# Kernel tuning notes

Hardware: AMD Instinct MI355X
Metric: run time of the kernel (lower is better)

Reference implementation:

```python
import jax, jax.numpy as jnp
import numpy as np

B, T, F_IN, L, D = 512, 32, 4096, 256, 256
EPS = 1e-8
KM_ITERS = 100


def _linear(x, w, b):
    return x @ w.T + b


def _clf(h, w0, b0, w1, b1, w2, b2, w3, b3):
    # Linear->ReLU (Dropout is identity in eval) x3 then final Linear
    h = jax.nn.relu(_linear(h, w0, b0))
    h = jax.nn.relu(_linear(h, w1, b1))
    h = jax.nn.relu(_linear(h, w2, b2))
    return _linear(h, w3, b3)


def _kmeans_cosine(f):
    # f: (T, L). 2-cluster kmeans with cosine distance, fixed iteration count.
    fn = f / (jnp.linalg.norm(f, axis=1, keepdims=True) + EPS)
    centers0 = jnp.stack([f[0], f[T // 2]])  # deterministic init (ref: random pick)

    def step(centers, _):
        cn = centers / (jnp.linalg.norm(centers, axis=1, keepdims=True) + EPS)
        sim = fn @ cn.T                           # (T,2) cosine similarity
        assign = jnp.argmax(sim, axis=1)          # argmin of (1 - sim)
        mask = jax.nn.one_hot(assign, 2, dtype=f.dtype)  # (T,2)
        counts = mask.sum(axis=0)                 # (2,)
        new = (mask.T @ f) / jnp.clip(counts, 1.0)[:, None]
        new = jnp.where(counts[:, None] > 0, new, centers)
        return new, assign

    centers, assigns = jax.lax.scan(step, centers0, None, length=KM_ITERS)
    return assigns[-1], centers


def setup_inputs() -> dict:
    key = jax.random.key(0)
    ks = jax.random.split(key, 32)
    s = 0.02
    inp = {
        "x": jax.random.normal(ks[0], (B, T, F_IN), dtype=jnp.float32),
        "tsn_w": jax.random.normal(ks[1], (L, F_IN, 3), dtype=jnp.float32) * s,
        "tsn_b": jnp.zeros((L,), jnp.float32),
        "aV_w": jax.random.normal(ks[2], (D, L), dtype=jnp.float32) * s,
        "aV_b": jnp.zeros((D,), jnp.float32),
        "aU_w": jax.random.normal(ks[3], (D, L), dtype=jnp.float32) * s,
        "aU_b": jnp.zeros((D,), jnp.float32),
        "gate_w": jax.random.normal(ks[4], (1, D), dtype=jnp.float32) * s,
        "gate_b": jnp.zeros((1,), jnp.float32),
    }
    dims_bag = [(D, L), (D // 2, D), (32, D // 2), (1, 32)]
    dims_seg = [(D, L + 1), (D // 2, D), (32, D // 2), (1, 32)]
    for j, (o, i) in enumerate(dims_bag):
        inp[f"cb_w{j}"] = jax.random.normal(ks[5 + j], (o, i), dtype=jnp.float32) * s
        inp[f"cb_b{j}"] = jnp.zeros((o,), jnp.float32)
    for j, (o, i) in enumerate(dims_seg):
        inp[f"cs_w{j}"] = jax.random.normal(ks[9 + j], (o, i), dtype=jnp.float32) * s
        inp[f"cs_b{j}"] = jnp.zeros((o,), jnp.float32)
    return inp


def reference(x, tsn_w, tsn_b, aV_w, aV_b, aU_w, aU_b, gate_w, gate_b,
              cb_w0, cb_b0, cb_w1, cb_b1, cb_w2, cb_b2, cb_w3, cb_b3,
              cs_w0, cs_b0, cs_w1, cs_b1, cs_w2, cs_b2, cs_w3, cs_b3):
    feat_in = jnp.nan_to_num(x)  # (B,T,4096)
    # Conv1d over time (kernel 3, pad 1): NCH layout
    feature = jax.lax.conv_general_dilated(
        feat_in.transpose(0, 2, 1), tsn_w, (1,), [(1, 1)],
        dimension_numbers=('NCH', 'OIH', 'NCH')) + tsn_b[None, :, None]
    feature = feature.transpose(0, 2, 1)  # (B,T,L)

    # Gated MIL attention
    A_V = jnp.tanh(_linear(feature, aV_w, aV_b))
    A_U = jax.nn.sigmoid(_linear(feature, aU_w, aU_b))
    A = _linear(A_V * A_U, gate_w, gate_b)      # (B,T,1)
    At = A.transpose(0, 2, 1)                   # (B,1,T)
    bag = jnp.einsum('bot,btl->bol', jax.nn.softmax(At, axis=2), feature)[:, 0]  # (B,L)

    output1 = jax.nn.sigmoid(_clf(bag, cb_w0, cb_b0, cb_w1, cb_b1,
                                  cb_w2, cb_b2, cb_w3, cb_b3)).reshape(-1)  # (B,)

    seg_in = jnp.concatenate([feature, A], axis=2)  # (B,T,L+1)
    output_seg = jax.nn.sigmoid(_clf(seg_in, cs_w0, cs_b0, cs_w1, cs_b1,
                                     cs_w2, cs_b2, cs_w3, cs_b3)[..., 0])  # (B,T)

    # Per-sample 2-means cosine clustering (batched via vmap instead of python loop)
    assigns, _ = jax.vmap(_kmeans_cosine)(feature)  # (B,T) int
    mask0 = assigns == 0
    cnt0 = mask0.sum(1).astype(output_seg.dtype)
    cnt1 = T - cnt0
    m0 = jnp.where(mask0, output_seg, 0.0).sum(1) / jnp.clip(cnt0, 1.0)
    m1 = jnp.where(~mask0, output_seg, 0.0).sum(1) / jnp.clip(cnt1, 1.0)
    m0 = jnp.where(cnt0 > 0, m0, -jnp.inf)
    m1 = jnp.where(cnt1 > 0, m1, -jnp.inf)
    output2 = jnp.maximum(m0, m1)  # (B,)

    weight = 0.5
    output = jnp.stack([output1 * weight, output2 * (1.0 - weight)], axis=1)  # (B,2)
    # (ragged cluster index lists replaced by the dense assignment map `assigns`)
    return feature, assigns, output_seg, output, At
```

## Files before the change

kernel.cpp:

```cpp
#include <hip/hip_runtime.h>
#include <cfloat>
#include <cmath>

#define NB 512
#define NT 32
#define FIN 4096
#define NL 256
#define ND 256
#define NM (NB*NT)
#define KCONV (3*FIN)
#define PLANE 3145728
#define KTILES 192

#define BM 128
#define BN 128
#define BK 32
#define LDT 132

typedef __attribute__((ext_vector_type(8))) short short8_t;
typedef __attribute__((ext_vector_type(4))) float f32x4;

__device__ __forceinline__ float sigmoidf_(float v) { return 1.0f / (1.0f + expf(-v)); }

__device__ __forceinline__ unsigned short f2bf(float v) {
  unsigned u = __float_as_uint(v);
  unsigned r = u + 0x7FFFu + ((u >> 16) & 1u);
  return (unsigned short)(r >> 16);
}
__device__ __forceinline__ float bf2f(unsigned short h) {
  return __uint_as_float(((unsigned)h) << 16);
}

__global__ void __launch_bounds__(256) repack_frag_k(const float* __restrict__ w,
                                                     unsigned short* __restrict__ wt) {
  int d = blockIdx.x * 256 + threadIdx.x;
  int kt = d >> 13;
  int bc = (d >> 9) & 15;
  int lane = (d >> 3) & 63;
  int j = d & 7;
  int kb = lane >> 4;
  int kk = kt * 32 + kb * 8 + j;
  int l = bc * 16 + (lane & 15);
  int tap = kk >> 12;
  int f = kk & 4095;
  float v = w[(size_t)l * KCONV + f * 3 + tap];
  unsigned short hi = f2bf(v);
  unsigned short lo = f2bf(v - bf2f(hi));
  wt[d] = hi;
  wt[PLANE + d] = lo;
}

__global__ void __launch_bounds__(256) repack_dense_k(const float* __restrict__ W1,
    const float* __restrict__ W2, int nsplit, int ldw, int KB, int N16,
    unsigned short* __restrict__ wt, int planeElems) {
  int d = blockIdx.x * 256 + threadIdx.x;
  if (d >= planeElems) return;
  int j = d & 7;
  int lane = (d >> 3) & 63;
  int bckt = d >> 9;
  int bc = bckt % N16;
  int kt = bckt / N16;
  int kk = kt * 32 + (lane >> 4) * 8 + j;
  int l = bc * 16 + (lane & 15);
  float v = 0.f;
  if (kk < KB) {
    if (l < nsplit) v = W1[(size_t)l * ldw + kk];
    else            v = W2[(size_t)(l - nsplit) * ldw + kk];
  }
  unsigned short hi = f2bf(v);
  unsigned short lo = f2bf(v - bf2f(hi));
  wt[d] = hi;
  wt[planeElems + d] = lo;
}

__global__ void __launch_bounds__(256) conv_mfma3_k(const float* __restrict__ x,
    const unsigned short* __restrict__ WT, float* __restrict__ PART) {
  __shared__ __align__(16) unsigned short LB[2][16384];
  const int tid = threadIdx.x;
  const int lane = tid & 63;
  const int w = tid >> 6;
  const int wr = w >> 1, wc = w & 1;
  const int bid = blockIdx.x;
  const int swz = ((bid & 7) << 6) + (bid >> 3);
  const int m0 = (swz & 127) << 7;
  const int by = (swz >> 7) & 1;
  const int kz = swz >> 8;
  const int ktBase = kz * KTILES;

  f32x4 acc[4][4] = {};
  float4 avA[4];

  auto loadA = [&](int kt, float4* av) {
#pragma unroll
    for (int rb = 0; rb < 2; ++rb) {
      const int br = (w << 1) + rb;
      const int gm = m0 + br * 16 + (lane & 15);
      const int tap = kt >> 7;
      const int f0 = (kt & 127) << 5;
      const int tt = (gm & 31) + tap - 1;
      if ((unsigned)tt < 32u) {
        const float* src = x + (size_t)(gm + tap - 1) * FIN + f0 + ((lane >> 4) << 3);
        av[rb*2+0] = *reinterpret_cast<const float4*>(src);
        av[rb*2+1] = *reinterpret_cast<const float4*>(src + 4);
      } else {
        av[rb*2+0] = make_float4(0.f,0.f,0.f,0.f);
        av[rb*2+1] = make_float4(0.f,0.f,0.f,0.f);
      }
    }
  };
  auto writeA = [&](int buf, const float4* av) {
#pragma unroll
    for (int rb = 0; rb < 2; ++rb) {
      float vv[8];
      *reinterpret_cast<float4*>(&vv[0]) = av[rb*2+0];
      *reinterpret_cast<float4*>(&vv[4]) = av[rb*2+1];
      __align__(16) unsigned short hi8[8];
      __align__(16) unsigned short lo8[8];
#pragma unroll
      for (int e = 0; e < 8; ++e) {
        float v = vv[e];
        v = (v == v) ? v : 0.0f;
        unsigned short h = f2bf(v);
        hi8[e] = h;
        lo8[e] = f2bf(v - bf2f(h));
      }
      const int br = (w << 1) + rb;
      const int off = (br << 9) + (lane << 3);
      *reinterpret_cast<short8_t*>(&LB[buf][off])        = *reinterpret_cast<const short8_t*>(hi8);
      *reinterpret_cast<short8_t*>(&LB[buf][4096 + off]) = *reinterpret_cast<const short8_t*>(lo8);
    }
  };
  auto stageB = [&](int buf, int kt) {
#pragma unroll
    for (int cb = 0; cb < 2; ++cb) {
      const int bc = (w << 1) + cb;
      const unsigned short* sh = WT + (((size_t)kt * 16 + (by << 3) + bc) << 9) + (lane << 3);
      __builtin_amdgcn_global_load_lds(
          (const __attribute__((address_space(1))) void*)sh,
          (__attribute__((address_space(3))) void*)&LB[buf][8192 + (bc << 9)], 16, 0, 0);
      __builtin_amdgcn_global_load_lds(
          (const __attribute__((address_space(1))) void*)(sh + PLANE),
          (__attribute__((address_space(3))) void*)&LB[buf][12288 + (bc << 9)], 16, 0, 0);
    }
  };

  stageB(0, ktBase);
  loadA(ktBase, avA);
  asm volatile("s_waitcnt vmcnt(0)" ::: "memory");
  writeA(0, avA);
  loadA(ktBase + 1, avA);
  stageB(1, ktBase + 1);
  asm volatile("s_waitcnt lgkmcnt(0)" ::: "memory");
  __builtin_amdgcn_s_barrier();

  for (int i = 0; i < KTILES; ++i) {
    const int cur = i & 1;
    if (i + 1 < KTILES) {
      asm volatile("s_waitcnt vmcnt(4)" ::: "memory");
      writeA(cur ^ 1, avA);
      if (i + 2 < KTILES) loadA(ktBase + i + 2, avA);
    }
    {
      const unsigned short* A0 = &LB[cur][0];
      const unsigned short* B0 = &LB[cur][8192];
      short8_t bh[4], bl[4];
#pragma unroll
      for (int c = 0; c < 4; ++c) {
        const int bc = wc * 4 + c;
        bh[c] = *reinterpret_cast<const short8_t*>(B0 + (bc << 9) + (lane << 3));
        bl[c] = *reinterpret_cast<const short8_t*>(B0 + 4096 + (bc << 9) + (lane << 3));
      }
#pragma unroll
      for (int r = 0; r < 4; ++r) {
        const int br = wr * 4 + r;
        short8_t ah = *reinterpret_cast<const short8_t*>(A0 + (br << 9) + (lane << 3));
        short8_t al = *reinterpret_cast<const short8_t*>(A0 + 4096 + (br << 9) + (lane << 3));
#pragma unroll
        for (int c = 0; c < 4; ++c) {
          acc[r][c] = __builtin_amdgcn_mfma_f32_16x16x32_bf16(ah, bh[c], acc[r][c], 0, 0, 0);
          acc[r][c] = __builtin_amdgcn_mfma_f32_16x16x32_bf16(ah, bl[c], acc[r][c], 0, 0, 0);
          acc[r][c] = __builtin_amdgcn_mfma_f32_16x16x32_bf16(al, bh[c], acc[r][c], 0, 0, 0);
        }
      }
    }
    if (i + 1 < KTILES) {
      if (i + 2 < KTILES) {
        asm volatile("s_waitcnt vmcnt(4)" ::: "memory");
      } else {
        asm volatile("s_waitcnt vmcnt(0)" ::: "memory");
      }
      asm volatile("s_waitcnt lgkmcnt(0)" ::: "memory");
      __builtin_amdgcn_sched_barrier(0);
      __builtin_amdgcn_s_barrier();
      if (i + 2 < KTILES) stageB(cur, ktBase + i + 2);
    }
  }

  float* P = PART + (size_t)kz * ((size_t)NM * NL);
#pragma unroll
  for (int r = 0; r < 4; ++r) {
#pragma unroll
    for (int c = 0; c < 4; ++c) {
#pragma unroll
      for (int e = 0; e < 4; ++e) {
        int row = m0 + wr * 64 + r * 16 + ((lane >> 4) << 2) + e;
        int col = by * 128 + wc * 64 + c * 16 + (lane & 15);
        P[(size_t)row * NL + col] = acc[r][c][e];
      }
    }
  }
}

__global__ void __launch_bounds__(256) reduce_bias_k(const float* __restrict__ PART,
    const float* __restrict__ bias, float* __restrict__ feat) {
  int i = blockIdx.x * 256 + threadIdx.x;
  size_t base = (size_t)i * 4;
  float4 a = *reinterpret_cast<const float4*>(PART + base);
  float4 b = *reinterpret_cast<const float4*>(PART + (size_t)NM * NL + base);
  int c0 = (int)(base & 255);
  float4 bb = *reinterpret_cast<const float4*>(bias + c0);
  float4 o;
  o.x = a.x + b.x + bb.x;
  o.y = a.y + b.y + bb.y;
  o.z = a.z + b.z + bb.z;
  o.w = a.w + b.w + bb.w;
  *reinterpret_cast<float4*>(feat + base) = o;
}

template <int ACT, int SEG>
__global__ void __launch_bounds__(256) mfma_gemm_k(const float* __restrict__ A, int lda,
    const float* __restrict__ Aws, const unsigned short* __restrict__ WT,
    int planeElems, int N16, int KT,
    const float* __restrict__ bias1, const float* __restrict__ bias2, int bsplit,
    float* __restrict__ C, int N) {
  __shared__ __align__(16) unsigned short AS[8192];
  __shared__ __align__(16) unsigned short BS[8192];
  const int tid = threadIdx.x;
  const int m0 = blockIdx.x * 128;
  const int by = blockIdx.y;
  const int lane = tid & 63;
  const int w = tid >> 6, wr = w >> 1, wc = w & 1;
  const int kb = tid & 3;
  const int rquot = tid >> 2;

  f32x4 acc[4][4] = {};
  float4 avreg[4];
  short8_t bvreg[4];

  {
#pragma unroll
    for (int u = 0; u < 2; ++u) {
      int gm = m0 + u * 64 + rquot;
      const float* src = A + (size_t)gm * lda + kb * 8;
      avreg[u*2+0] = *reinterpret_cast<const float4*>(src);
      avreg[u*2+1] = *reinterpret_cast<const float4*>(src + 4);
    }
#pragma unroll
    for (int q = 0; q < 4; ++q) {
      int p = q >> 1, pass = q & 1;
      bvreg[q] = *reinterpret_cast<const short8_t*>(WT + (size_t)p * planeElems
                  + ((size_t)by * 8) * 512 + (pass*256 + tid) * 8);
    }
  }

  for (int i = 0; i < KT; ++i) {
#pragma unroll
    for (int u = 0; u < 2; ++u) {
      float vv[8];
      *reinterpret_cast<float4*>(&vv[0]) = avreg[u*2+0];
      *reinterpret_cast<float4*>(&vv[4]) = avreg[u*2+1];
      __align__(16) unsigned short hi[8];
      __align__(16) unsigned short lo[8];
#pragma unroll
      for (int e = 0; e < 8; ++e) {
        float v = vv[e];
        unsigned short h = f2bf(v);
        hi[e] = h;
        lo[e] = f2bf(v - bf2f(h));
      }
      int row = u * 64 + rquot;
      int br = row >> 4;
      int lanew = (row & 15) + (kb << 4);
      int off = br * 512 + lanew * 8;
      *reinterpret_cast<short8_t*>(AS + off)        = *reinterpret_cast<const short8_t*>(hi);
      *reinterpret_cast<short8_t*>(AS + 4096 + off) = *reinterpret_cast<const short8_t*>(lo);
    }
#pragma unroll
    for (int q = 0; q < 4; ++q) {
      int p = q >> 1, pass = q & 1;
      *reinterpret_cast<short8_t*>(BS + p * 4096 + (pass*256 + tid) * 8) = bvreg[q];
    }
    __syncthreads();

    if (i + 1 < KT) {
      int kk0 = (i + 1) * 32;
#pragma unroll
      for (int u = 0; u < 2; ++u) {
        int gm = m0 + u * 64 + rquot;
        if (SEG && kk0 >= 256) {
          float a0 = (kb == 0) ? Aws[gm] : 0.f;
          avreg[u*2+0] = make_float4(a0, 0.f, 0.f, 0.f);
          avreg[u*2+1] = make_float4(0.f, 0.f, 0.f, 0.f);
        } else {
          const float* src = A + (size_t)gm * lda + kk0 + kb * 8;
          avreg[u*2+0] = *reinterpret_cast<const float4*>(src);
          avreg[u*2+1] = *reinterpret_cast<const float4*>(src + 4);
        }
      }
#pragma unroll
      for (int q = 0; q < 4; ++q) {
        int p = q >> 1, pass = q & 1;
        bvreg[q] = *reinterpret_cast<const short8_t*>(WT + (size_t)p * planeElems
                    + ((size_t)(i + 1) * N16 + by * 8) * 512 + (pass*256 + tid) * 8);
      }
    }

    short8_t bh[4], bl[4];
#pragma unroll
    for (int c = 0; c < 4; ++c) {
      int bc = wc * 4 + c;
      bh[c] = *reinterpret_cast<const short8_t*>(BS + bc * 512 + lane * 8);
      bl[c] = *reinterpret_cast<const short8_t*>(BS + 4096 + bc * 512 + lane * 8);
    }
#pragma unroll
    for (int r = 0; r < 4; ++r) {
      int br = wr * 4 + r;
      short8_t ah = *reinterpret_cast<const short8_t*>(AS + br * 512 + lane * 8);
      short8_t al = *reinterpret_cast<const short8_t*>(AS + 4096 + br * 512 + lane * 8);
#pragma unroll
      for (int c = 0; c < 4; ++c) {
        acc[r][c] = __builtin_amdgcn_mfma_f32_16x16x32_bf16(ah, bh[c], acc[r][c], 0, 0, 0);
        acc[r][c] = __builtin_amdgcn_mfma_f32_16x16x32_bf16(ah, bl[c], acc[r][c], 0, 0, 0);
        acc[r][c] = __builtin_amdgcn_mfma_f32_16x16x32_bf16(al, bh[c], acc[r][c], 0, 0, 0);
      }
    }
    __syncthreads();
  }

#pragma unroll
  for (int r = 0; r < 4; ++r) {
#pragma unroll
    for (int c = 0; c < 4; ++c) {
#pragma unroll
      for (int e = 0; e < 4; ++e) {
        int row = m0 + wr * 64 + r * 16 + ((lane >> 4) << 2) + e;
        int col = by * 128 + wc * 64 + c * 16 + (lane & 15);
        float b = (col < bsplit) ? bias1[col] : bias2[col - bsplit];
        float v = acc[r][c][e] + b;
        if (ACT == 1) v = fmaxf(v, 0.f);
        C[(size_t)row * N + col] = v;
      }
    }
  }
}

template <int ACT>
__global__ void __launch_bounds__(256) gemm_wt_k(const float* __restrict__ A, int lda,
    const float* __restrict__ W, int ldw, int KB,
    const float* __restrict__ bias, float* __restrict__ C,
    int N, int K) {
  __shared__ float As[BK][LDT];
  __shared__ float Bs[BK][LDT];
  const int tid = threadIdx.x;
  const int m0 = blockIdx.x * BM;
  const int n0 = blockIdx.y * BN;
  const int row0 = (tid >> 4) << 3;
  const int col0 = (tid & 15) << 3;
  float acc[8][8] = {};
  for (int kk0 = 0; kk0 < K; kk0 += BK) {
#pragma unroll
    for (int i = 0; i < 4; ++i) {
      int v = i * 256 + tid;
      int row = v >> 3;
      int f4 = (v & 7) << 2;
      float4 val = *reinterpret_cast<const float4*>(A + (size_t)(m0 + row) * lda + kk0 + f4);
      As[f4 + 0][row] = val.x;
      As[f4 + 1][row] = val.y;
      As[f4 + 2][row] = val.z;
      As[f4 + 3][row] = val.w;
    }
#pragma unroll
    for (int i = 0; i < 4; ++i) {
      int v = i * 256 + tid;
      int n = v >> 3;
      int kq = (v & 7) << 2;
      int gn = n0 + n;
#pragma unroll
      for (int j = 0; j < 4; ++j) {
        int kk = kk0 + kq + j;
        float bv = 0.f;
        if (gn < N && kk < KB) bv = W[(size_t)gn * ldw + kk];
        Bs[kq + j][n] = bv;
      }
    }
    __syncthreads();
#pragma unroll
    for (int kk = 0; kk < BK; ++kk) {
      float a[8], b[8];
      *reinterpret_cast<float4*>(&a[0]) = *reinterpret_cast<const float4*>(&As[kk][row0]);
      *reinterpret_cast<float4*>(&a[4]) = *reinterpret_cast<const float4*>(&As[kk][row0 + 4]);
      *reinterpret_cast<float4*>(&b[0]) = *reinterpret_cast<const float4*>(&Bs[kk][col0]);
      *reinterpret_cast<float4*>(&b[4]) = *reinterpret_cast<const float4*>(&Bs[kk][col0 + 4]);
#pragma unroll
      for (int r = 0; r < 8; ++r)
#pragma unroll
        for (int c = 0; c < 8; ++c)
          acc[r][c] = fmaf(a[r], b[c], acc[r][c]);
    }
    __syncthreads();
  }
#pragma unroll
  for (int r = 0; r < 8; ++r) {
    int m = m0 + row0 + r;
#pragma unroll
    for (int c = 0; c < 8; ++c) {
      int n = n0 + col0 + c;
      if (n < N) {
        float v = acc[r][c] + bias[n];
        if (ACT == 1) v = fmaxf(v, 0.f);
        C[(size_t)m * (size_t)N + n] = v;
      }
    }
  }
}

__global__ void __launch_bounds__(256) gate_k(const float* __restrict__ Y,
    const float* __restrict__ gw, const float* __restrict__ gb,
    float* __restrict__ Aws, float* __restrict__ At) {
  int lane = threadIdx.x & 63;
  int m = blockIdx.x * 4 + (threadIdx.x >> 6);
  float4 v4 = *reinterpret_cast<const float4*>(Y + (size_t)m * 512 + lane * 4);
  float4 u4 = *reinterpret_cast<const float4*>(Y + (size_t)m * 512 + 256 + lane * 4);
  float4 g4 = *reinterpret_cast<const float4*>(gw + lane * 4);
  float s = tanhf(v4.x) * sigmoidf_(u4.x) * g4.x
          + tanhf(v4.y) * sigmoidf_(u4.y) * g4.y
          + tanhf(v4.z) * sigmoidf_(u4.z) * g4.z
          + tanhf(v4.w) * sigmoidf_(u4.w) * g4.w;
#pragma unroll
  for (int off = 32; off > 0; off >>= 1) s += __shfl_xor(s, off, 64);
  if (lane == 0) {
    float a = s + gb[0];
    Aws[m] = a;
    At[m] = a;
  }
}

__global__ void __launch_bounds__(256) softmax_bag_k(const float* __restrict__ Aws,
    const float* __restrict__ feat, float* __restrict__ bag) {
  __shared__ float av[NT];
  __shared__ float ev[NT];
  int b = blockIdx.x, tid = threadIdx.x;
  if (tid < NT) av[tid] = Aws[b * NT + tid];
  __syncthreads();
  float mx = -FLT_MAX;
#pragma unroll
  for (int t = 0; t < NT; ++t) mx = fmaxf(mx, av[t]);
  if (tid < NT) ev[tid] = expf(av[tid] - mx);
  __syncthreads();
  float ssum = 0.f;
#pragma unroll
  for (int t = 0; t < NT; ++t) ssum += ev[t];
  float accv = 0.f;
#pragma unroll
  for (int t = 0; t < NT; ++t) accv += ev[t] * feat[((size_t)b * NT + t) * NL + tid];
  bag[(size_t)b * NL + tid] = accv / ssum;
}

__global__ void __launch_bounds__(256) rowdot32_k(const float* __restrict__ H,
    const float* __restrict__ w, const float* __restrict__ bptr,
    float* __restrict__ outp, int ostride, float scale) {
  int m = blockIdx.x * 256 + threadIdx.x;
  const float* h = H + (size_t)m * 32;
  float s = bptr[0];
#pragma unroll
  for (int i = 0; i < 32; i += 4) {
    float4 hv = *reinterpret_cast<const float4*>(h + i);
    float4 wv = *reinterpret_cast<const float4*>(w + i);
    s += hv.x * wv.x + hv.y * wv.y + hv.z * wv.z + hv.w * wv.w;
  }
  outp[(size_t)m * ostride] = scale * sigmoidf_(s);
}

__global__ void __launch_bounds__(64) kmeans_k(const float* __restrict__ feat,
    const float* __restrict__ seg, float* __restrict__ assigns_out,
    float* __restrict__ outpair) {
  __shared__ float fls[NT][260];
  int b = blockIdx.x, lane = threadIdx.x;
  int l0 = lane << 2;
  float fn[NT][4];
#pragma unroll
  for (int t = 0; t < NT; ++t) {
    float4 v = *reinterpret_cast<const float4*>(feat + ((size_t)b * NT + t) * NL + l0);
    *reinterpret_cast<float4*>(&fls[t][l0]) = v;
    float ss = v.x * v.x + v.y * v.y + v.z * v.z + v.w * v.w;
#pragma unroll
    for (int off = 32; off > 0; off >>= 1) ss += __shfl_xor(ss, off, 64);
    float nr = sqrtf(ss) + 1e-8f;
    fn[t][0] = v.x / nr; fn[t][1] = v.y / nr; fn[t][2] = v.z / nr; fn[t][3] = v.w / nr;
  }
  __syncthreads();
  float cr0[4], cr1[4];
#pragma unroll
  for (int i = 0; i < 4; ++i) { cr0[i] = fls[0][l0 + i]; cr1[i] = fls[16][l0 + i]; }

  unsigned long long amask = 0ull;
  unsigned long long prev = ~0ull;
  int c1n = 0;
  for (int it = 0; it < 100; ++it) {
    float ss0 = cr0[0]*cr0[0] + cr0[1]*cr0[1] + cr0[2]*cr0[2] + cr0[3]*cr0[3];
    float ss1 = cr1[0]*cr1[0] + cr1[1]*cr1[1] + cr1[2]*cr1[2] + cr1[3]*cr1[3];
#pragma unroll
    for (int off = 32; off > 0; off >>= 1) {
      ss0 += __shfl_xor(ss0, off, 64);
      ss1 += __shfl_xor(ss1, off, 64);
    }
    float nr0 = sqrtf(ss0) + 1e-8f, nr1 = sqrtf(ss1) + 1e-8f;
    float cn0[4], cn1[4];
#pragma unroll
    for (int i = 0; i < 4; ++i) { cn0[i] = cr0[i] / nr0; cn1[i] = cr1[i] / nr1; }
    float p[64];
#pragma unroll
    for (int t = 0; t < NT; ++t) {
      p[2*t]   = fn[t][0]*cn0[0] + fn[t][1]*cn0[1] + fn[t][2]*cn0[2] + fn[t][3]*cn0[3];
      p[2*t+1] = fn[t][0]*cn1[0] + fn[t][1]*cn1[1] + fn[t][2]*cn1[2] + fn[t][3]*cn1[3];
    }
    float v32[32];
    { bool hi = (lane & 32) != 0;
#pragma unroll
      for (int i = 0; i < 32; ++i) {
        float keep = hi ? p[32+i] : p[i];
        float send = hi ? p[i] : p[32+i];
        v32[i] = keep + __shfl_xor(send, 32, 64);
      } }
    float v16[16];
    { bool hi = (lane & 16) != 0;
#pragma unroll
      for (int i = 0; i < 16; ++i) {
        float keep = hi ? v32[16+i] : v32[i];
        float send = hi ? v32[i] : v32[16+i];
        v16[i] = keep + __shfl_xor(send, 16, 64);
      } }
    float v8[8];
    { bool hi = (lane & 8) != 0;
#pragma unroll
      for (int i = 0; i < 8; ++i) {
        float keep = hi ? v16[8+i] : v16[i];
        float send = hi ? v16[i] : v16[8+i];
        v8[i] = keep + __shfl_xor(send, 8, 64);
      } }
    float v4[4];
    { bool hi = (lane & 4) != 0;
#pragma unroll
      for (int i = 0; i < 4; ++i) {
        float keep = hi ? v8[4+i] : v8[i];
        float send = hi ? v8[i] : v8[4+i];
        v4[i] = keep + __shfl_xor(send, 4, 64);
      } }
    float v2[2];
    { bool hi = (lane & 2) != 0;
#pragma unroll
      for (int i = 0; i < 2; ++i) {
        float keep = hi ? v4[2+i] : v4[i];
        float send = hi ? v4[i] : v4[2+i];
        v2[i] = keep + __shfl_xor(send, 2, 64);
      } }
    float sim;
    { bool hi = (lane & 1) != 0;
      float keep = hi ? v2[1] : v2[0];
      float send = hi ? v2[0] : v2[1];
      sim = keep + __shfl_xor(send, 1, 64);
    }
    float simo = __shfl_xor(sim, 1, 64);
    bool is0 = (lane & 1) == 0;
    unsigned long long mask = __ballot(is0 && (simo > sim));
    int c1 = __popcll(mask);
    int c0 = NT - c1;
    amask = mask; c1n = c1;
    if (mask == prev) break;
    prev = mask;
    float s0v[4] = {0,0,0,0}, s1v[4] = {0,0,0,0};
#pragma unroll
    for (int t = 0; t < NT; ++t) {
      float mt = (float)((mask >> (2*t)) & 1ull);
      float nt = 1.0f - mt;
      float4 fv = *reinterpret_cast<const float4*>(&fls[t][l0]);
      s1v[0] = fmaf(mt, fv.x, s1v[0]); s1v[1] = fmaf(mt, fv.y, s1v[1]);
      s1v[2] = fmaf(mt, fv.z, s1v[2]); s1v[3] = fmaf(mt, fv.w, s1v[3]);
      s0v[0] = fmaf(nt, fv.x, s0v[0]); s0v[1] = fmaf(nt, fv.y, s0v[1]);
      s0v[2] = fmaf(nt, fv.z, s0v[2]); s0v[3] = fmaf(nt, fv.w, s0v[3]);
    }
    float fc0 = fmaxf((float)c0, 1.0f), fc1 = fmaxf((float)c1, 1.0f);
#pragma unroll
    for (int i = 0; i < 4; ++i) {
      float n0v = s0v[i] / fc0;
      float n1v = s1v[i] / fc1;
      cr0[i] = (c0 > 0) ? n0v : cr0[i];
      cr1[i] = (c1 > 0) ? n1v : cr1[i];
    }
  }
  if (lane < NT)
    assigns_out[(size_t)b * NT + lane] = (amask & (1ull << (2*lane))) ? 1.0f : 0.0f;
  if (lane == 0) {
    float sum0 = 0.f, sum1 = 0.f;
    for (int t = 0; t < NT; ++t) {
      float sv = seg[(size_t)b * NT + t];
      if (amask & (1ull << (2*t))) sum1 += sv; else sum0 += sv;
    }
    int c1 = c1n, c0 = NT - c1n;
    float m0 = (c0 > 0) ? (sum0 / fmaxf((float)c0, 1.f)) : -INFINITY;
    float m1 = (c1 > 0) ? (sum1 / fmaxf((float)c1, 1.f)) : -INFINITY;
    outpair[(size_t)b * 2 + 1] = 0.5f * fmaxf(m0, m1);
  }
}

extern "C" void kernel_launch(void* const* d_in, const int* in_sizes, int n_in,
                              void* d_out, int out_size, void* d_ws, size_t ws_size,
                              hipStream_t stream) {
  const float* x      = (const float*)d_in[0];
  const float* tsn_w  = (const float*)d_in[1];
  const float* tsn_b  = (const float*)d_in[2];
  const float* aV_w   = (const float*)d_in[3];
  const float* aV_b   = (const float*)d_in[4];
  const float* aU_w   = (const float*)d_in[5];
  const float* aU_b   = (const float*)d_in[6];
  const float* gate_w = (const float*)d_in[7];
  const float* gate_b = (const float*)d_in[8];
  const float* cb_w0  = (const float*)d_in[9];
  const float* cb_b0  = (const float*)d_in[10];
  const float* cb_w1  = (const float*)d_in[11];
  const float* cb_b1  = (const float*)d_in[12];
  const float* cb_w2  = (const float*)d_in[13];
  const float* cb_b2  = (const float*)d_in[14];
  const float* cb_w3  = (const float*)d_in[15];
  const float* cb_b3  = (const float*)d_in[16];
  const float* cs_w0  = (const float*)d_in[17];
  const float* cs_b0  = (const float*)d_in[18];
  const float* cs_w1  = (const float*)d_in[19];
  const float* cs_b1  = (const float*)d_in[20];
  const float* cs_w2  = (const float*)d_in[21];
  const float* cs_b2  = (const float*)d_in[22];
  const float* cs_w3  = (const float*)d_in[23];
  const float* cs_b3  = (const float*)d_in[24];

  float* out = (float*)d_out;
  float* o_feat   = out;
  float* o_assign = out + 4194304;
  float* o_seg    = out + 4210688;
  float* o_out    = out + 4227072;
  float* o_At     = out + 4228096;

  char* ws = (char*)d_ws;
  unsigned short* WT = (unsigned short*)ws;
  float* PART  = (float*)(ws + 12582912);
  unsigned short* WVU = (unsigned short*)ws;
  unsigned short* WC0 = (unsigned short*)(ws + 524288);
  unsigned short* WC1 = (unsigned short*)(ws + 819200);
  float* AWS   = (float*)(ws + 950272);
  float* BAG   = (float*)(ws + 1015808);
  float* BH0   = (float*)(ws + 1540096);
  float* BH1   = (float*)(ws + 2064384);
  float* BH2   = (float*)(ws + 2326528);
  float* Y     = (float*)(ws + 12582912);
  float* SH0   = (float*)(ws + 12582912);
  float* SH1   = (float*)(ws + 29360128);
  float* SH2   = (float*)(ws + 37748736);

  repack_frag_k<<<dim3(12288), dim3(256), 0, stream>>>(tsn_w, WT);
  conv_mfma3_k<<<dim3(512), dim3(256), 0, stream>>>(x, WT, PART);
  reduce_bias_k<<<dim3(4096), dim3(256), 0, stream>>>(PART, tsn_b, o_feat);
  repack_dense_k<<<dim3(512), dim3(256), 0, stream>>>(aV_w, aU_w, 256, 256, 256, 32, WVU, 131072);
  repack_dense_k<<<dim3(288), dim3(256), 0, stream>>>(cs_w0, cs_w0, 256, 257, 257, 16, WC0, 73728);
  repack_dense_k<<<dim3(128), dim3(256), 0, stream>>>(cs_w1, cs_w1, 256, 256, 256, 8, WC1, 32768);
  mfma_gemm_k<0,0><<<dim3(128, 4), dim3(256), 0, stream>>>(o_feat, 256, nullptr, WVU,
      131072, 32, 8, aV_b, aU_b, 256, Y, 512);
  gate_k<<<dim3(4096), dim3(256), 0, stream>>>(Y, gate_w, gate_b, AWS, o_At);
  softmax_bag_k<<<dim3(512), dim3(256), 0, stream>>>(AWS, o_feat, BAG);
  gemm_wt_k<1><<<dim3(4, 2), dim3(256), 0, stream>>>(BAG, 256, cb_w0, 256, 256, cb_b0, BH0, 256, 256);
  gemm_wt_k<1><<<dim3(4, 1), dim3(256), 0, stream>>>(BH0, 256, cb_w1, 256, 256, cb_b1, BH1, 128, 256);
  gemm_wt_k<1><<<dim3(4, 1), dim3(256), 0, stream>>>(BH1, 128, cb_w2, 128, 128, cb_b2, BH2, 32, 128);
  rowdot32_k<<<dim3(2), dim3(256), 0, stream>>>(BH2, cb_w3, cb_b3, o_out, 2, 0.5f);
  mfma_gemm_k<1,1><<<dim3(128, 2), dim3(256), 0, stream>>>(o_feat, 256, AWS, WC0,
      73728, 16, 9, cs_b0, cs_b0, 256, SH0, 256);
  mfma_gemm_k<1,0><<<dim3(128, 1), dim3(256), 0, stream>>>(SH0, 256, nullptr, WC1,
      32768, 8, 8, cs_b1, cs_b1, 128, SH1, 128);
  gemm_wt_k<1><<<dim3(128, 1), dim3(256), 0, stream>>>(SH1, 128, cs_w2, 128, 128, cs_b2, SH2, 32, 128);
  rowdot32_k<<<dim3(64), dim3(256), 0, stream>>>(SH2, cs_w3, cs_b3, o_seg, 1, 1.0f);
  kmeans_k<<<dim3(512), dim3(64), 0, stream>>>(o_feat, o_seg, o_assign, o_out);
}
```

Baseline: 736.1 us.

## Replace LDS-staged conv GEMM with register-direct double-buffered loads

```diff
diff --git a/kernel.cpp b/kernel.cpp
--- a/kernel.cpp
+++ b/kernel.cpp
@@ -73,127 +73,91 @@
   wt[planeElems + d] = lo;
 }
 
-__global__ void __launch_bounds__(256) conv_mfma3_k(const float* __restrict__ x,
+struct Aset { float4 v[8]; };
+struct Bset { short8_t b[8]; };
+
+__device__ __forceinline__ void conv_loadstep(const float* __restrict__ x,
+    const unsigned short* __restrict__ WT, int m0, int by, int kt,
+    int wr, int wc, int lane, Aset& A, Bset& B) {
+  const int tap = kt >> 7;
+  const int fbase = ((kt & 127) << 5) + ((lane >> 4) << 3);
+#pragma unroll
+  for (int r = 0; r < 4; ++r) {
+    const int br = wr * 4 + r;
+    const int gm = m0 + br * 16 + (lane & 15);
+    const int tt = (gm & 31) + tap - 1;
+    float4 a0 = make_float4(0.f, 0.f, 0.f, 0.f);
+    float4 a1 = a0;
+    if ((unsigned)tt < 32u) {
+      const float* src = x + (size_t)(gm + tap - 1) * FIN + fbase;
+      a0 = *reinterpret_cast<const float4*>(src);
+      a1 = *reinterpret_cast<const float4*>(src + 4);
+    }
+    A.v[2*r]   = a0;
+    A.v[2*r+1] = a1;
+  }
+  const unsigned short* bbase = WT + (((size_t)kt * 16 + (by << 3)) << 9) + (lane << 3);
+#pragma unroll
+  for (int c = 0; c < 4; ++c) {
+    const int bc = wc * 4 + c;
+    B.b[c]     = *reinterpret_cast<const short8_t*>(bbase + ((size_t)bc << 9));
+    B.b[4 + c] = *reinterpret_cast<const short8_t*>(bbase + ((size_t)bc << 9) + PLANE);
+  }
+}
+
+__device__ __forceinline__ void conv_compstep(const Aset& A, const Bset& B,
+                                              f32x4 acc[4][4]) {
+#pragma unroll
+  for (int r = 0; r < 4; ++r) {
+    float vv[8];
+    *reinterpret_cast<float4*>(&vv[0]) = A.v[2*r];
+    *reinterpret_cast<float4*>(&vv[4]) = A.v[2*r+1];
+    __align__(16) unsigned short hi8[8];
+    __align__(16) unsigned short lo8[8];
+#pragma unroll
+    for (int e = 0; e < 8; ++e) {
+      float v = vv[e];
+      v = (v == v) ? v : 0.0f;
+      unsigned short h = f2bf(v);
+      hi8[e] = h;
+      lo8[e] = f2bf(v - bf2f(h));
+    }
+    short8_t ah = *reinterpret_cast<const short8_t*>(hi8);
+    short8_t al = *reinterpret_cast<const short8_t*>(lo8);
+#pragma unroll
+    for (int c = 0; c < 4; ++c) {
+      acc[r][c] = __builtin_amdgcn_mfma_f32_16x16x32_bf16(ah, B.b[c],     acc[r][c], 0, 0, 0);
+      acc[r][c] = __builtin_amdgcn_mfma_f32_16x16x32_bf16(ah, B.b[4 + c], acc[r][c], 0, 0, 0);
+      acc[r][c] = __builtin_amdgcn_mfma_f32_16x16x32_bf16(al, B.b[c],     acc[r][c], 0, 0, 0);
+    }
+  }
+}
+
+__global__ void __launch_bounds__(256) conv_mfma4_k(const float* __restrict__ x,
     const unsigned short* __restrict__ WT, float* __restrict__ PART) {
-  __shared__ __align__(16) unsigned short LB[2][16384];
   const int tid = threadIdx.x;
   const int lane = tid & 63;
   const int w = tid >> 6;
   const int wr = w >> 1, wc = w & 1;
   const int bid = blockIdx.x;
-  const int swz = ((bid & 7) << 6) + (bid >> 3);
-  const int m0 = (swz & 127) << 7;
-  const int by = (swz >> 7) & 1;
-  const int kz = swz >> 8;
+  const int xcd = bid & 7;
+  const int j = bid >> 3;
+  const int m0 = (xcd * 16 + (j >> 2)) << 7;
+  const int by = j & 1;
+  const int kz = (j >> 1) & 1;
   const int ktBase = kz * KTILES;
 
   f32x4 acc[4][4] = {};
-  float4 avA[4];
-
-  auto loadA = [&](int kt, float4* av) {
-#pragma unroll
-    for (int rb = 0; rb < 2; ++rb) {
-      const int br = (w << 1) + rb;
-      const int gm = m0 + br * 16 + (lane & 15);
-      const int tap = kt >> 7;
-      const int f0 = (kt & 127) << 5;
-      const int tt = (gm & 31) + tap - 1;
-      if ((unsigned)tt < 32u) {
-        const float* src = x + (size_t)(gm + tap - 1) * FIN + f0 + ((lane >> 4) << 3);
-        av[rb*2+0] = *reinterpret_cast<const float4*>(src);
-        av[rb*2+1] = *reinterpret_cast<const float4*>(src + 4);
-      } else {
-        av[rb*2+0] = make_float4(0.f,0.f,0.f,0.f);
-        av[rb*2+1] = make_float4(0.f,0.f,0.f,0.f);
-      }
-    }
-  };
-  auto writeA = [&](int buf, const float4* av) {
-#pragma unroll
-    for (int rb = 0; rb < 2; ++rb) {
-      float vv[8];
-      *reinterpret_cast<float4*>(&vv[0]) = av[rb*2+0];
-      *reinterpret_cast<float4*>(&vv[4]) = av[rb*2+1];
-      __align__(16) unsigned short hi8[8];
-      __align__(16) unsigned short lo8[8];
-#pragma unroll
-      for (int e = 0; e < 8; ++e) {
-        float v = vv[e];
-        v = (v == v) ? v : 0.0f;
-        unsigned short h = f2bf(v);
-        hi8[e] = h;
-        lo8[e] = f2bf(v - bf2f(h));
-      }
-      const int br = (w << 1) + rb;
-      const int off = (br << 9) + (lane << 3);
-      *reinterpret_cast<short8_t*>(&LB[buf][off])        = *reinterpret_cast<const short8_t*>(hi8);
-      *reinterpret_cast<short8_t*>(&LB[buf][4096 + off]) = *reinterpret_cast<const short8_t*>(lo8);
-    }
-  };
-  auto stageB = [&](int buf, int kt) {
-#pragma unroll
-    for (int cb = 0; cb < 2; ++cb) {
-      const int bc = (w << 1) + cb;
-      const unsigned short* sh = WT + (((size_t)kt * 16 + (by << 3) + bc) << 9) + (lane << 3);
-      __builtin_amdgcn_global_load_lds(
-          (const __attribute__((address_space(1))) void*)sh,
-          (__attribute__((address_space(3))) void*)&LB[buf][8192 + (bc << 9)], 16, 0, 0);
-      __builtin_amdgcn_global_load_lds(
-          (const __attribute__((address_space(1))) void*)(sh + PLANE),
-          (__attribute__((address_space(3))) void*)&LB[buf][12288 + (bc << 9)], 16, 0, 0);
-    }
-  };
-
-  stageB(0, ktBase);
-  loadA(ktBase, avA);
-  asm volatile("s_waitcnt vmcnt(0)" ::: "memory");
-  writeA(0, avA);
-  loadA(ktBase + 1, avA);
-  stageB(1, ktBase + 1);
-  asm volatile("s_waitcnt lgkmcnt(0)" ::: "memory");
-  __builtin_amdgcn_s_barrier();
-
-  for (int i = 0; i < KTILES; ++i) {
-    const int cur = i & 1;
-    if (i + 1 < KTILES) {
-      asm volatile("s_waitcnt vmcnt(4)" ::: "memory");
-      writeA(cur ^ 1, avA);
-      if (i + 2 < KTILES) loadA(ktBase + i + 2, avA);
-    }
-    {
-      const unsigned short* A0 = &LB[cur][0];
-      const unsigned short* B0 = &LB[cur][8192];
-      short8_t bh[4], bl[4];
-#pragma unroll
-      for (int c = 0; c < 4; ++c) {
-        const int bc = wc * 4 + c;
-        bh[c] = *reinterpret_cast<const short8_t*>(B0 + (bc << 9) + (lane << 3));
-        bl[c] = *reinterpret_cast<const short8_t*>(B0 + 4096 + (bc << 9) + (lane << 3));
-      }
-#pragma unroll
-      for (int r = 0; r < 4; ++r) {
-        const int br = wr * 4 + r;
-        short8_t ah = *reinterpret_cast<const short8_t*>(A0 + (br << 9) + (lane << 3));
-        short8_t al = *reinterpret_cast<const short8_t*>(A0 + 4096 + (br << 9) + (lane << 3));
-#pragma unroll
-        for (int c = 0; c < 4; ++c) {
-          acc[r][c] = __builtin_amdgcn_mfma_f32_16x16x32_bf16(ah, bh[c], acc[r][c], 0, 0, 0);
-          acc[r][c] = __builtin_amdgcn_mfma_f32_16x16x32_bf16(ah, bl[c], acc[r][c], 0, 0, 0);
-          acc[r][c] = __builtin_amdgcn_mfma_f32_16x16x32_bf16(al, bh[c], acc[r][c], 0, 0, 0);
-        }
-      }
-    }
-    if (i + 1 < KTILES) {
-      if (i + 2 < KTILES) {
-        asm volatile("s_waitcnt vmcnt(4)" ::: "memory");
-      } else {
-        asm volatile("s_waitcnt vmcnt(0)" ::: "memory");
-      }
-      asm volatile("s_waitcnt lgkmcnt(0)" ::: "memory");
-      __builtin_amdgcn_sched_barrier(0);
-      __builtin_amdgcn_s_barrier();
-      if (i + 2 < KTILES) stageB(cur, ktBase + i + 2);
-    }
+  Aset A0, A1;
+  Bset B0, B1;
+
+  conv_loadstep(x, WT, m0, by, ktBase, wr, wc, lane, A0, B0);
+  for (int i = 0; i < KTILES; i += 2) {
+    conv_loadstep(x, WT, m0, by, ktBase + i + 1, wr, wc, lane, A1, B1);
+    conv_compstep(A0, B0, acc);
+    if (i + 2 < KTILES)
+      conv_loadstep(x, WT, m0, by, ktBase + i + 2, wr, wc, lane, A0, B0);
+    conv_compstep(A1, B1, acc);
   }
 
   float* P = PART + (size_t)kz * ((size_t)NM * NL);
@@ -666,7 +630,7 @@
   float* SH2   = (float*)(ws + 37748736);
 
   repack_frag_k<<<dim3(12288), dim3(256), 0, stream>>>(tsn_w, WT);
-  conv_mfma3_k<<<dim3(512), dim3(256), 0, stream>>>(x, WT, PART);
+  conv_mfma4_k<<<dim3(512), dim3(256), 0, stream>>>(x, WT, PART);
   reduce_bias_k<<<dim3(4096), dim3(256), 0, stream>>>(PART, tsn_b, o_feat);
   repack_dense_k<<<dim3(512), dim3(256), 0, stream>>>(aV_w, aU_w, 256, 256, 256, 32, WVU, 131072);
   repack_dense_k<<<dim3(288), dim3(256), 0, stream>>>(cs_w0, cs_w0, 256, 257, 257, 16, WC0, 73728);
```

Result: slower. 851.9 us (+15.7%).

## Widen conv GEMM tile to full 256 columns with 512-thread blocks

Applied to the files above, without the earlier changes.

```diff
diff --git a/kernel.cpp b/kernel.cpp
--- a/kernel.cpp
+++ b/kernel.cpp
@@ -73,138 +73,129 @@
   wt[planeElems + d] = lo;
 }
 
-__global__ void __launch_bounds__(256) conv_mfma3_k(const float* __restrict__ x,
+__global__ void __launch_bounds__(512) conv_mfma6_k(const float* __restrict__ x,
     const unsigned short* __restrict__ WT, float* __restrict__ PART) {
-  __shared__ __align__(16) unsigned short LB[2][16384];
+  __shared__ __align__(16) unsigned short LB[2][24576];
   const int tid = threadIdx.x;
   const int lane = tid & 63;
   const int w = tid >> 6;
   const int wr = w >> 1, wc = w & 1;
   const int bid = blockIdx.x;
-  const int swz = ((bid & 7) << 6) + (bid >> 3);
-  const int m0 = (swz & 127) << 7;
-  const int by = (swz >> 7) & 1;
-  const int kz = swz >> 8;
+  const int xcd = bid & 7;
+  const int j = bid >> 3;
+  const int m0 = (xcd * 16 + (j >> 1)) << 7;
+  const int kz = j & 1;
   const int ktBase = kz * KTILES;
-
-  f32x4 acc[4][4] = {};
-  float4 avA[4];
-
-  auto loadA = [&](int kt, float4* av) {
-#pragma unroll
-    for (int rb = 0; rb < 2; ++rb) {
-      const int br = (w << 1) + rb;
-      const int gm = m0 + br * 16 + (lane & 15);
-      const int tap = kt >> 7;
-      const int f0 = (kt & 127) << 5;
-      const int tt = (gm & 31) + tap - 1;
-      if ((unsigned)tt < 32u) {
-        const float* src = x + (size_t)(gm + tap - 1) * FIN + f0 + ((lane >> 4) << 3);
-        av[rb*2+0] = *reinterpret_cast<const float4*>(src);
-        av[rb*2+1] = *reinterpret_cast<const float4*>(src + 4);
-      } else {
-        av[rb*2+0] = make_float4(0.f,0.f,0.f,0.f);
-        av[rb*2+1] = make_float4(0.f,0.f,0.f,0.f);
-      }
+  const int ar = tid >> 2;
+  const int akc = tid & 3;
+
+  f32x4 acc[2][8] = {};
+  float4 avA[2];
+
+  auto loadA = [&](int kt) {
+    const int tap = kt >> 7;
+    const int f0 = (kt & 127) << 5;
+    const int gm = m0 + ar;
+    const int tt = (gm & 31) + tap - 1;
+    if ((unsigned)tt < 32u) {
+      const float* src = x + (size_t)(gm + tap - 1) * FIN + f0 + (akc << 3);
+      avA[0] = *reinterpret_cast<const float4*>(src);
+      avA[1] = *reinterpret_cast<const float4*>(src + 4);
+    } else {
+      avA[0] = make_float4(0.f, 0.f, 0.f, 0.f);
+      avA[1] = make_float4(0.f, 0.f, 0.f, 0.f);
     }
   };
-  auto writeA = [&](int buf, const float4* av) {
-#pragma unroll
-    for (int rb = 0; rb < 2; ++rb) {
-      float vv[8];
-      *reinterpret_cast<float4*>(&vv[0]) = av[rb*2+0];
-      *reinterpret_cast<float4*>(&vv[4]) = av[rb*2+1];
-      __align__(16) unsigned short hi8[8];
-      __align__(16) unsigned short lo8[8];
-#pragma unroll
-      for (int e = 0; e < 8; ++e) {
-        float v = vv[e];
-        v = (v == v) ? v : 0.0f;
-        unsigned short h = f2bf(v);
-        hi8[e] = h;
-        lo8[e] = f2bf(v - bf2f(h));
-      }
-      const int br = (w << 1) + rb;
-      const int off = (br << 9) + (lane << 3);
-      *reinterpret_cast<short8_t*>(&LB[buf][off])        = *reinterpret_cast<const short8_t*>(hi8);
-      *reinterpret_cast<short8_t*>(&LB[buf][4096 + off]) = *reinterpret_cast<const short8_t*>(lo8);
-    }
+  auto writeA = [&](int buf) {
+    float vv[8];
+    *reinterpret_cast<float4*>(&vv[0]) = avA[0];
+    *reinterpret_cast<float4*>(&vv[4]) = avA[1];
+    __align__(16) unsigned short hi8[8];
+    __align__(16) unsigned short lo8[8];
+#pragma unroll
+    for (int e = 0; e < 8; ++e) {
+      float v = vv[e];
+      v = (v == v) ? v : 0.0f;
+      unsigned short h = f2bf(v);
+      hi8[e] = h;
+      lo8[e] = f2bf(v - bf2f(h));
+    }
+    const int off = ((ar >> 4) << 9) + (((ar & 15) + (akc << 4)) << 3);
+    *reinterpret_cast<short8_t*>(&LB[buf][off])        = *reinterpret_cast<const short8_t*>(hi8);
+    *reinterpret_cast<short8_t*>(&LB[buf][4096 + off]) = *reinterpret_cast<const short8_t*>(lo8);
   };
   auto stageB = [&](int buf, int kt) {
 #pragma unroll
-    for (int cb = 0; cb < 2; ++cb) {
-      const int bc = (w << 1) + cb;
-      const unsigned short* sh = WT + (((size_t)kt * 16 + (by << 3) + bc) << 9) + (lane << 3);
+    for (int q = 0; q < 4; ++q) {
+      const int c = w + (q << 3);
+      const int p = c >> 4, bc = c & 15;
+      const unsigned short* src = WT + (size_t)p * PLANE
+          + (((size_t)kt * 16 + bc) << 9) + (lane << 3);
       __builtin_amdgcn_global_load_lds(
-          (const __attribute__((address_space(1))) void*)sh,
-          (__attribute__((address_space(3))) void*)&LB[buf][8192 + (bc << 9)], 16, 0, 0);
-      __builtin_amdgcn_global_load_lds(
-          (const __attribute__((address_space(1))) void*)(sh + PLANE),
-          (__attribute__((address_space(3))) void*)&LB[buf][12288 + (bc << 9)], 16, 0, 0);
+          (const __attribute__((address_space(1))) void*)src,
+          (__attribute__((address_space(3))) void*)&LB[buf][8192 + (p << 13) + (bc << 9)],
+          16, 0, 0);
     }
   };
 
+  loadA(ktBase);
   stageB(0, ktBase);
-  loadA(ktBase, avA);
   asm volatile("s_waitcnt vmcnt(0)" ::: "memory");
-  writeA(0, avA);
-  loadA(ktBase + 1, avA);
-  stageB(1, ktBase + 1);
+  writeA(0);
+  __builtin_amdgcn_sched_barrier(0);
   asm volatile("s_waitcnt lgkmcnt(0)" ::: "memory");
   __builtin_amdgcn_s_barrier();
 
   for (int i = 0; i < KTILES; ++i) {
     const int cur = i & 1;
     if (i + 1 < KTILES) {
-      asm volatile("s_waitcnt vmcnt(4)" ::: "memory");
-      writeA(cur ^ 1, avA);
-      if (i + 2 < KTILES) loadA(ktBase + i + 2, avA);
-    }
+      loadA(ktBase + i + 1);
+      stageB(cur ^ 1, ktBase + i + 1);
+      asm volatile("s_waitcnt vmcnt(6)" ::: "memory");
+    } else {
+      asm volatile("s_waitcnt vmcnt(0)" ::: "memory");
+    }
+    __builtin_amdgcn_sched_barrier(0);
+    __builtin_amdgcn_s_barrier();
+
     {
       const unsigned short* A0 = &LB[cur][0];
       const unsigned short* B0 = &LB[cur][8192];
-      short8_t bh[4], bl[4];
-#pragma unroll
-      for (int c = 0; c < 4; ++c) {
-        const int bc = wc * 4 + c;
+      short8_t bh[8], bl[8];
+#pragma unroll
+      for (int c = 0; c < 8; ++c) {
+        const int bc = (wc << 3) + c;
         bh[c] = *reinterpret_cast<const short8_t*>(B0 + (bc << 9) + (lane << 3));
-        bl[c] = *reinterpret_cast<const short8_t*>(B0 + 4096 + (bc << 9) + (lane << 3));
-      }
-#pragma unroll
-      for (int r = 0; r < 4; ++r) {
-        const int br = wr * 4 + r;
+        bl[c] = *reinterpret_cast<const short8_t*>(B0 + 8192 + (bc << 9) + (lane << 3));
+      }
+#pragma unroll
+      for (int r = 0; r < 2; ++r) {
+        const int br = (wr << 1) + r;
         short8_t ah = *reinterpret_cast<const short8_t*>(A0 + (br << 9) + (lane << 3));
         short8_t al = *reinterpret_cast<const short8_t*>(A0 + 4096 + (br << 9) + (lane << 3));
 #pragma unroll
-        for (int c = 0; c < 4; ++c) {
+        for (int c = 0; c < 8; ++c) {
           acc[r][c] = __builtin_amdgcn_mfma_f32_16x16x32_bf16(ah, bh[c], acc[r][c], 0, 0, 0);
           acc[r][c] = __builtin_amdgcn_mfma_f32_16x16x32_bf16(ah, bl[c], acc[r][c], 0, 0, 0);
           acc[r][c] = __builtin_amdgcn_mfma_f32_16x16x32_bf16(al, bh[c], acc[r][c], 0, 0, 0);
         }
       }
     }
-    if (i + 1 < KTILES) {
-      if (i + 2 < KTILES) {
-        asm volatile("s_waitcnt vmcnt(4)" ::: "memory");
-      } else {
-        asm volatile("s_waitcnt vmcnt(0)" ::: "memory");
-      }
-      asm volatile("s_waitcnt lgkmcnt(0)" ::: "memory");
-      __builtin_amdgcn_sched_barrier(0);
-      __builtin_amdgcn_s_barrier();
-      if (i + 2 < KTILES) stageB(cur, ktBase + i + 2);
-    }
+    if (i + 1 < KTILES) writeA(cur ^ 1);
+    __builtin_amdgcn_sched_barrier(0);
+    asm volatile("s_waitcnt lgkmcnt(0)" ::: "memory");
+    __builtin_amdgcn_s_barrier();
   }
 
   float* P = PART + (size_t)kz * ((size_t)NM * NL);
 #pragma unroll
-  for (int r = 0; r < 4; ++r) {
-#pragma unroll
-    for (int c = 0; c < 4; ++c) {
+  for (int r = 0; r < 2; ++r) {
+#pragma unroll
+    for (int c = 0; c < 8; ++c) {
 #pragma unroll
       for (int e = 0; e < 4; ++e) {
-        int row = m0 + wr * 64 + r * 16 + ((lane >> 4) << 2) + e;
-        int col = by * 128 + wc * 64 + c * 16 + (lane & 15);
+        int row = m0 + ((wr << 1) + r) * 16 + ((lane >> 4) << 2) + e;
+        int col = (wc << 7) + c * 16 + (lane & 15);
         P[(size_t)row * NL + col] = acc[r][c][e];
       }
     }
@@ -666,7 +657,7 @@
   float* SH2   = (float*)(ws + 37748736);
 
   repack_frag_k<<<dim3(12288), dim3(256), 0, stream>>>(tsn_w, WT);
-  conv_mfma3_k<<<dim3(512), dim3(256), 0, stream>>>(x, WT, PART);
+  conv_mfma6_k<<<dim3(256), dim3(512), 0, stream>>>(x, WT, PART);
   reduce_bias_k<<<dim3(4096), dim3(256), 0, stream>>>(PART, tsn_b, o_feat);
   repack_dense_k<<<dim3(512), dim3(256), 0, stream>>>(aV_w, aU_w, 256, 256, 256, 32, WVU, 131072);
   repack_dense_k<<<dim3(288), dim3(256), 0, stream>>>(cs_w0, cs_w0, 256, 257, 257, 16, WC0, 73728);
```

After: 709.6 us. -3.6%, faster.
